# Optimization experiments

Hardware: AMD Instinct MI355X
Metric: run time of the kernel (lower is better)

The kernel has to match this reference:

```python
import jax, jax.numpy as jnp
import numpy as np

K1 = 3                      # spline kernel size per pseudo dim
SIZE = float(np.sqrt(2.0))  # pseudo_cartesian normalization size


def spline_weights(p, k):
    """Degree-1 open B-spline basis over 2D pseudo coords.
    p: [..., 2] in [0,1]. Returns basis [..., 4], weight_index [..., 4]."""
    v = jnp.clip(p, 0.0, 1.0) * (k - 1)
    lo = jnp.floor(v)
    frac = v - lo
    lo = lo.astype(jnp.int32)
    off = jnp.array([0, 1], dtype=jnp.int32)
    w0 = jnp.stack([1.0 - frac[..., 0], frac[..., 0]], axis=-1)   # [...,2]
    w1 = jnp.stack([1.0 - frac[..., 1], frac[..., 1]], axis=-1)   # [...,2]
    i0 = jnp.clip(lo[..., 0:1] + off, 0, k - 1)                    # [...,2]
    i1 = jnp.clip(lo[..., 1:2] + off, 0, k - 1)                    # [...,2]
    basis = (w0[..., :, None] * w1[..., None, :]).reshape(*p.shape[:-1], 4)
    widx = (i0[..., :, None] + k * i1[..., None, :]).reshape(*p.shape[:-1], 4)
    return basis, widx


def setup_inputs() -> dict:
    key = jax.random.key(0)
    kx, ke, kp, kq, kw, kb = jax.random.split(key, 6)
    N, C, P, E, K = 50000, 64, 16, 800000, K1 * K1
    x = jax.random.normal(kx, (N, C), dtype=jnp.float32)
    pos = jax.random.uniform(kp, (N, 2), dtype=jnp.float32)
    pose = jax.random.normal(kq, (N, P, 2), dtype=jnp.float32)
    pose = pose / (jnp.linalg.norm(pose, axis=-1, keepdims=True) + 1e-8)  # unit pose vectors
    W = jax.random.normal(kw, (P, K, C), dtype=jnp.float32) / np.sqrt(C * 4.0)
    bias = jax.random.normal(kb, (P,), dtype=jnp.float32) * 0.01
    edge_index = jax.random.randint(ke, (2, E), 0, N, dtype=jnp.int64)
    return {"x": x, "pos": pos, "pose": pose, "W": W, "bias": bias,
            "edge_index": edge_index}


def reference(x, pos, pose, W, bias, edge_index):
    N, C = x.shape
    P = pose.shape[1]
    row, col = edge_index[0], edge_index[1]
    # pseudo_cartesian: normalized relative position in [0,1]^2
    pseudo = (pos[col] - pos[row]) / (2.0 * SIZE) + 0.5              # [E,2]
    # posevec_to_rotmat on detached pose vectors
    pose_c = jax.lax.stop_gradient(pose)
    a, b = pose_c[..., 0], pose_c[..., 1]
    R = jnp.stack([jnp.stack([a, -b], -1), jnp.stack([b, a], -1)], -2)  # [N,P,2,2]
    Re = R[row]                                                      # [E,P,2,2]
    # rotate pseudo coords about (0.5, 0.5), batched over all poses
    p = jnp.einsum('epij,ej->epi', Re, pseudo - 0.5) + 0.5           # [E,P,2]
    basis, widx = spline_weights(p, K1)                              # [E,P,4]
    # SplineConv (out_channels=1, no root weight, no norm):
    # precompute per-node per-pose per-kernel-bin projections
    Z = jnp.einsum('nc,pkc->npk', x, W)                              # [N,P,K]
    pidx = jnp.arange(P)[None, :, None]
    vals = Z[col[:, None, None], pidx, widx]                         # [E,P,4]
    msg = jnp.sum(basis * vals, axis=-1)                             # [E,P]
    out = jax.ops.segment_sum(msg, row, num_segments=N)              # [N,P]
    return out + bias[None, :]
```

## Files before the change

kernel.cpp:

```cpp
#include <hip/hip_runtime.h>
#include <hip/hip_bf16.h>

#define C_DIM 64
#define P_DIM 16
#define K_DIM 9
#define PK (P_DIM * K_DIM)
#define INV2S 0.35355339059327373f

#define ZS_STRIDE 152
#define SH_FLOATS 4864

__global__ __launch_bounds__(256) void z_gemm_kernel(const float* __restrict__ x,
                                                     const float* __restrict__ W,
                                                     const float* __restrict__ bias,
                                                     float* __restrict__ out,
                                                     __hip_bfloat16* __restrict__ Zb,
                                                     int N) {
    __shared__ float sh_raw[SH_FLOATS];
    float (*xs)[C_DIM + 4] = (float(*)[C_DIM + 4])sh_raw;
    __hip_bfloat16* zs = (__hip_bfloat16*)sh_raw;

    const int block_row = blockIdx.x * 64;
    const int tid = threadIdx.x;

    {
        const float4 b4 = ((const float4*)bias)[tid & 3];
        const int o4 = block_row * 4 + tid;
        if (o4 < N * 4) ((float4*)out)[o4] = b4;
    }

    for (int i = tid; i < C_DIM * (C_DIM / 4); i += 256) {
        int r = i >> 4, c4 = i & 15;
        int gr = block_row + r;
        float4 v = make_float4(0.0f, 0.0f, 0.0f, 0.0f);
        if (gr < N) v = ((const float4*)x)[(size_t)gr * (C_DIM / 4) + c4];
        *(float4*)&xs[r][c4 * 4] = v;
    }
    __syncthreads();

    const int rg = tid & 15;
    const int p  = tid >> 4;
    const int j0 = p * K_DIM;

    float acc[4][K_DIM];
    #pragma unroll
    for (int i = 0; i < 4; ++i)
        #pragma unroll
        for (int k = 0; k < K_DIM; ++k) acc[i][k] = 0.0f;

    const float4* W4 = (const float4*)W;
    #pragma unroll 4
    for (int cs = 0; cs < 16; ++cs) {
        float4 xv[4];
        #pragma unroll
        for (int i = 0; i < 4; ++i) xv[i] = *(const float4*)&xs[rg + 16 * i][cs * 4];
        #pragma unroll
        for (int k = 0; k < K_DIM; ++k) {
            float4 wv = W4[(size_t)(j0 + k) * (C_DIM / 4) + cs];
            #pragma unroll
            for (int i = 0; i < 4; ++i) {
                acc[i][k] = fmaf(xv[i].x, wv.x, acc[i][k]);
                acc[i][k] = fmaf(xv[i].y, wv.y, acc[i][k]);
                acc[i][k] = fmaf(xv[i].z, wv.z, acc[i][k]);
                acc[i][k] = fmaf(xv[i].w, wv.w, acc[i][k]);
            }
        }
    }
    __syncthreads();

    #pragma unroll
    for (int i = 0; i < 4; ++i) {
        __hip_bfloat16* zrow = &zs[(rg + 16 * i) * ZS_STRIDE + j0];
        #pragma unroll
        for (int k = 0; k < K_DIM; ++k)
            zrow[k] = __float2bfloat16(acc[i][k]);
    }
    __syncthreads();

    const int nrow = min(64, N - block_row);
    float4* Zb4 = (float4*)Zb;
    for (int i = tid; i < nrow * 18; i += 256) {
        int row = i / 18, q = i - row * 18;
        float4 v = *(const float4*)&zs[row * ZS_STRIDE + q * 8];
        Zb4[(size_t)(block_row + row) * 18 + q] = v;
    }
}

#define EILP 8
__global__ __launch_bounds__(256) void edge_kernel(const int* __restrict__ ei,
                                                   const float* __restrict__ pos,
                                                   const float* __restrict__ pose,
                                                   const __hip_bfloat16* __restrict__ Zb,
                                                   float* __restrict__ out,
                                                   int E) {
    const int p  = threadIdx.x & 15;
    const int eg = threadIdx.x >> 4;
    const int e0 = blockIdx.x * (16 * EILP) + eg;

    int  r[EILP], c[EILP];
    bool valid[EILP];
    #pragma unroll
    for (int it = 0; it < EILP; ++it) {
        int e = e0 + it * 16;
        valid[it] = (e < E);
        int ec = valid[it] ? e : 0;
        r[it] = ei[ec];
        c[it] = ei[E + ec];
    }

    float d0[EILP], d1[EILP];
    #pragma unroll
    for (int it = 0; it < EILP; ++it) {
        const float2 pc = ((const float2*)pos)[c[it]];
        const float2 pr = ((const float2*)pos)[r[it]];
        d0[it] = (pc.x - pr.x) * INV2S;
        d1[it] = (pc.y - pr.y) * INV2S;
    }

    float2 ab[EILP];
    #pragma unroll
    for (int it = 0; it < EILP; ++it)
        ab[it] = ((const float2*)pose)[(size_t)r[it] * P_DIM + p];

    #pragma unroll
    for (int it = 0; it < EILP; ++it) {
        const float p0 = fmaf(ab[it].x, d0[it], fmaf(-ab[it].y, d1[it], 0.5f));
        const float p1 = fmaf(ab[it].y, d0[it], fmaf( ab[it].x, d1[it], 0.5f));

        const float v0 = fminf(fmaxf(p0, 0.0f), 1.0f) * 2.0f;
        const float v1 = fminf(fmaxf(p1, 0.0f), 1.0f) * 2.0f;
        const float lo0 = floorf(v0);
        const float lo1 = floorf(v1);
        const float f0 = v0 - lo0;
        const float f1 = v1 - lo1;
        const int i00 = min((int)lo0, 2);
        const int i01 = min((int)lo0 + 1, 2);
        const int i10 = min((int)lo1, 2);
        const int i11 = min((int)lo1 + 1, 2);

        const __hip_bfloat16* __restrict__ Zp = Zb + (size_t)c[it] * PK + p * K_DIM;
        const float w00 = (1.0f - f0) * (1.0f - f1);
        const float w01 = (1.0f - f0) * f1;
        const float w10 = f0 * (1.0f - f1);
        const float w11 = f0 * f1;

        float m = w00 * __bfloat162float(Zp[i00 + 3 * i10]);
        m = fmaf(w01, __bfloat162float(Zp[i00 + 3 * i11]), m);
        m = fmaf(w10, __bfloat162float(Zp[i01 + 3 * i10]), m);
        m = fmaf(w11, __bfloat162float(Zp[i01 + 3 * i11]), m);

        if (valid[it]) atomicAdd(&out[(size_t)r[it] * P_DIM + p], m);
    }
}

extern "C" void kernel_launch(void* const* d_in, const int* in_sizes, int n_in,
                              void* d_out, int out_size, void* d_ws, size_t ws_size,
                              hipStream_t stream) {
    const float* x    = (const float*)d_in[0];
    const float* pos  = (const float*)d_in[1];
    const float* pose = (const float*)d_in[2];
    const float* W    = (const float*)d_in[3];
    const float* bias = (const float*)d_in[4];
    const int*   ei   = (const int*)d_in[5];

    const int N = in_sizes[0] / C_DIM;
    const int E = in_sizes[5] / 2;

    float* out = (float*)d_out;
    __hip_bfloat16* Zb = (__hip_bfloat16*)d_ws;

    z_gemm_kernel<<<(N + 63) / 64, 256, 0, stream>>>(x, W, bias, out, Zb, N);
    edge_kernel<<<(E + 16 * EILP - 1) / (16 * EILP), 256, 0, stream>>>(ei, pos, pose, Zb, out, E);
}
```

Before: 156.3 us.

## Repack Z as paired bf16 bins, precompute edge deltas, compress pose to bf16

```diff
diff --git a/kernel.cpp b/kernel.cpp
--- a/kernel.cpp
+++ b/kernel.cpp
@@ -4,21 +4,30 @@
 #define C_DIM 64
 #define P_DIM 16
 #define K_DIM 9
-#define PK (P_DIM * K_DIM)
 #define INV2S 0.35355339059327373f
 
-#define ZS_STRIDE 152
-#define SH_FLOATS 4864
+#define ZP_ROW 96
+#define ZP_STRIDE 100
+#define SH_FLOATS 6400
+
+__device__ __forceinline__ unsigned bf_bits(float x) {
+    unsigned u = __float_as_uint(x);
+    return (u + 0x7fffu + ((u >> 16) & 1u)) >> 16;
+}
+__device__ __forceinline__ float bf_lo(unsigned w) { return __uint_as_float(w << 16); }
+__device__ __forceinline__ float bf_hi(unsigned w) { return __uint_as_float(w & 0xffff0000u); }
 
 __global__ __launch_bounds__(256) void z_gemm_kernel(const float* __restrict__ x,
                                                      const float* __restrict__ W,
                                                      const float* __restrict__ bias,
+                                                     const float* __restrict__ pose,
                                                      float* __restrict__ out,
-                                                     __hip_bfloat16* __restrict__ Zb,
+                                                     unsigned* __restrict__ Zp,
+                                                     unsigned* __restrict__ poseb,
                                                      int N) {
     __shared__ float sh_raw[SH_FLOATS];
     float (*xs)[C_DIM + 4] = (float(*)[C_DIM + 4])sh_raw;
-    __hip_bfloat16* zs = (__hip_bfloat16*)sh_raw;
+    unsigned* zs = (unsigned*)sh_raw;
 
     const int block_row = blockIdx.x * 64;
     const int tid = threadIdx.x;
@@ -27,6 +36,17 @@
         const float4 b4 = ((const float4*)bias)[tid & 3];
         const int o4 = block_row * 4 + tid;
         if (o4 < N * 4) ((float4*)out)[o4] = b4;
+    }
+
+    #pragma unroll
+    for (int j = 0; j < 4; ++j) {
+        int idx = j * 256 + tid;
+        int gr = block_row + (idx >> 4);
+        int pp = idx & 15;
+        if (gr < N) {
+            float2 ab = ((const float2*)pose)[(size_t)gr * P_DIM + pp];
+            poseb[(size_t)gr * P_DIM + pp] = bf_bits(ab.x) | (bf_bits(ab.y) << 16);
+        }
     }
 
     for (int i = tid; i < C_DIM * (C_DIM / 4); i += 256) {
@@ -70,86 +90,99 @@
 
     #pragma unroll
     for (int i = 0; i < 4; ++i) {
-        __hip_bfloat16* zrow = &zs[(rg + 16 * i) * ZS_STRIDE + j0];
-        #pragma unroll
-        for (int k = 0; k < K_DIM; ++k)
-            zrow[k] = __float2bfloat16(acc[i][k]);
+        unsigned* zrow = &zs[(rg + 16 * i) * ZP_STRIDE + p];
+        #pragma unroll
+        for (int i1 = 0; i1 < 3; ++i1)
+            #pragma unroll
+            for (int b0 = 0; b0 < 2; ++b0)
+                zrow[(i1 * 2 + b0) * 16] =
+                    bf_bits(acc[i][b0 + 3 * i1]) | (bf_bits(acc[i][b0 + 1 + 3 * i1]) << 16);
     }
     __syncthreads();
 
     const int nrow = min(64, N - block_row);
-    float4* Zb4 = (float4*)Zb;
-    for (int i = tid; i < nrow * 18; i += 256) {
-        int row = i / 18, q = i - row * 18;
-        float4 v = *(const float4*)&zs[row * ZS_STRIDE + q * 8];
-        Zb4[(size_t)(block_row + row) * 18 + q] = v;
-    }
-}
-
-#define EILP 8
-__global__ __launch_bounds__(256) void edge_kernel(const int* __restrict__ ei,
+    float4* Zp4 = (float4*)Zp;
+    const float4* zs4 = (const float4*)sh_raw;
+    for (int i = tid; i < nrow * 24; i += 256) {
+        int row = i / 24, q = i - row * 24;
+        Zp4[(size_t)(block_row + row) * 24 + q] = zs4[row * (ZP_STRIDE / 4) + q];
+    }
+}
+
+__global__ __launch_bounds__(256) void prep_kernel(const int* __restrict__ ei,
                                                    const float* __restrict__ pos,
-                                                   const float* __restrict__ pose,
-                                                   const __hip_bfloat16* __restrict__ Zb,
+                                                   float4* __restrict__ prep,
+                                                   int E) {
+    int i = blockIdx.x * 256 + threadIdx.x;
+    if (i >= E) return;
+    const int r = ei[i];
+    const int c = ei[E + i];
+    const float2 pc = ((const float2*)pos)[c];
+    const float2 pr = ((const float2*)pos)[r];
+    prep[i] = make_float4((pc.x - pr.x) * INV2S, (pc.y - pr.y) * INV2S,
+                          __int_as_float(r), __int_as_float(c));
+}
+
+#define EILP 4
+__global__ __launch_bounds__(256) void edge_kernel(const float4* __restrict__ prep,
+                                                   const unsigned* __restrict__ poseb,
+                                                   const unsigned* __restrict__ Zp,
                                                    float* __restrict__ out,
                                                    int E) {
     const int p  = threadIdx.x & 15;
     const int eg = threadIdx.x >> 4;
     const int e0 = blockIdx.x * (16 * EILP) + eg;
 
-    int  r[EILP], c[EILP];
+    float4 ed[EILP];
     bool valid[EILP];
     #pragma unroll
     for (int it = 0; it < EILP; ++it) {
         int e = e0 + it * 16;
         valid[it] = (e < E);
-        int ec = valid[it] ? e : 0;
-        r[it] = ei[ec];
-        c[it] = ei[E + ec];
-    }
-
-    float d0[EILP], d1[EILP];
-    #pragma unroll
-    for (int it = 0; it < EILP; ++it) {
-        const float2 pc = ((const float2*)pos)[c[it]];
-        const float2 pr = ((const float2*)pos)[r[it]];
-        d0[it] = (pc.x - pr.x) * INV2S;
-        d1[it] = (pc.y - pr.y) * INV2S;
-    }
-
-    float2 ab[EILP];
-    #pragma unroll
-    for (int it = 0; it < EILP; ++it)
-        ab[it] = ((const float2*)pose)[(size_t)r[it] * P_DIM + p];
-
-    #pragma unroll
-    for (int it = 0; it < EILP; ++it) {
-        const float p0 = fmaf(ab[it].x, d0[it], fmaf(-ab[it].y, d1[it], 0.5f));
-        const float p1 = fmaf(ab[it].y, d0[it], fmaf( ab[it].x, d1[it], 0.5f));
-
-        const float v0 = fminf(fmaxf(p0, 0.0f), 1.0f) * 2.0f;
-        const float v1 = fminf(fmaxf(p1, 0.0f), 1.0f) * 2.0f;
+        ed[it] = prep[valid[it] ? e : 0];
+    }
+
+    unsigned pw[EILP];
+    #pragma unroll
+    for (int it = 0; it < EILP; ++it) {
+        int r = __float_as_int(ed[it].z);
+        pw[it] = poseb[(size_t)r * P_DIM + p];
+    }
+
+    unsigned pa[EILP], pb[EILP];
+    float f0[EILP], f1[EILP];
+    #pragma unroll
+    for (int it = 0; it < EILP; ++it) {
+        const float a = bf_lo(pw[it]);
+        const float b = bf_hi(pw[it]);
+        const float d0 = ed[it].x, d1 = ed[it].y;
+        const float p0 = fmaf(a, d0, fmaf(-b, d1, 0.5f));
+        const float p1 = fmaf(b, d0, fmaf( a, d1, 0.5f));
+
+        const float v0 = fminf(fmaxf(p0, 0.0f) * 2.0f, 1.9999999f);
+        const float v1 = fminf(fmaxf(p1, 0.0f) * 2.0f, 1.9999999f);
         const float lo0 = floorf(v0);
         const float lo1 = floorf(v1);
-        const float f0 = v0 - lo0;
-        const float f1 = v1 - lo1;
-        const int i00 = min((int)lo0, 2);
-        const int i01 = min((int)lo0 + 1, 2);
-        const int i10 = min((int)lo1, 2);
-        const int i11 = min((int)lo1 + 1, 2);
-
-        const __hip_bfloat16* __restrict__ Zp = Zb + (size_t)c[it] * PK + p * K_DIM;
-        const float w00 = (1.0f - f0) * (1.0f - f1);
-        const float w01 = (1.0f - f0) * f1;
-        const float w10 = f0 * (1.0f - f1);
-        const float w11 = f0 * f1;
-
-        float m = w00 * __bfloat162float(Zp[i00 + 3 * i10]);
-        m = fmaf(w01, __bfloat162float(Zp[i00 + 3 * i11]), m);
-        m = fmaf(w10, __bfloat162float(Zp[i01 + 3 * i10]), m);
-        m = fmaf(w11, __bfloat162float(Zp[i01 + 3 * i11]), m);
-
-        if (valid[it]) atomicAdd(&out[(size_t)r[it] * P_DIM + p], m);
+        f0[it] = v0 - lo0;
+        f1[it] = v1 - lo1;
+        const int b0 = (int)lo0;
+        const int b1 = (int)lo1;
+
+        const int c = __float_as_int(ed[it].w);
+        const unsigned* Zr = Zp + (size_t)c * ZP_ROW + b0 * 16 + p + b1 * 32;
+        pa[it] = Zr[0];
+        pb[it] = Zr[32];
+    }
+
+    #pragma unroll
+    for (int it = 0; it < EILP; ++it) {
+        const float za = bf_lo(pa[it]), zb = bf_hi(pa[it]);
+        const float zc = bf_lo(pb[it]), zd = bf_hi(pb[it]);
+        const float mlo = fmaf(f0[it], zb - za, za);
+        const float mhi = fmaf(f0[it], zd - zc, zc);
+        const float m   = fmaf(f1[it], mhi - mlo, mlo);
+        const int r = __float_as_int(ed[it].z);
+        if (valid[it]) atomicAdd(&out[(size_t)r * P_DIM + p], m);
     }
 }
 
@@ -167,8 +200,14 @@
     const int E = in_sizes[5] / 2;
 
     float* out = (float*)d_out;
-    __hip_bfloat16* Zb = (__hip_bfloat16*)d_ws;
-
-    z_gemm_kernel<<<(N + 63) / 64, 256, 0, stream>>>(x, W, bias, out, Zb, N);
-    edge_kernel<<<(E + 16 * EILP - 1) / (16 * EILP), 256, 0, stream>>>(ei, pos, pose, Zb, out, E);
-}
+
+    const size_t zp_bytes = (size_t)N * ZP_ROW * sizeof(unsigned);
+    const size_t pb_bytes = (size_t)N * P_DIM * sizeof(unsigned);
+    unsigned* Zp    = (unsigned*)d_ws;
+    unsigned* poseb = (unsigned*)((char*)d_ws + zp_bytes);
+    float4*   prep  = (float4*)((char*)d_ws + zp_bytes + pb_bytes);
+
+    z_gemm_kernel<<<(N + 63) / 64, 256, 0, stream>>>(x, W, bias, pose, out, Zp, poseb, N);
+    prep_kernel<<<(E + 255) / 256, 256, 0, stream>>>(ei, pos, prep, E);
+    edge_kernel<<<(E + 16 * EILP - 1) / (16 * EILP), 256, 0, stream>>>(prep, poseb, Zp, out, E);
+}
```

New measurement: 174.2 us. 11.4% more time.
